# Kernel tuning notes

Measured on AMD Instinct MI355X. Metric: run time of the kernel, lower is better.

Reference implementation:

```python
import jax, jax.numpy as jnp
import numpy as np

NUM_NODES = 50000
EMB_DIM = 128
PROJ_DIM = 768
HIDDEN = 256
NUM_REL = 16
NUM_BASES = 2
NUM_LAYERS = 3
NUM_EDGES = 400000
BN_EPS = 1e-5


def setup_inputs() -> dict:
    key = jax.random.key(0)
    ks = jax.random.split(key, 32)
    inp = {}
    inp["edge_index"] = jax.random.randint(ks[0], (2, NUM_EDGES), 0, NUM_NODES)
    inp["edge_type"] = jax.random.randint(ks[1], (NUM_EDGES,), 0, NUM_REL)
    inp["emb"] = jax.random.normal(ks[2], (NUM_NODES, EMB_DIM), jnp.float32)
    inp["proj_w"] = jax.random.normal(ks[3], (EMB_DIM, PROJ_DIM), jnp.float32) * 0.02
    inp["proj_b"] = jnp.zeros((PROJ_DIM,), jnp.float32)
    dims_in = [PROJ_DIM, HIDDEN, HIDDEN]
    for l in range(NUM_LAYERS):
        d_in = dims_in[l]
        k0, k1, k2 = jax.random.split(ks[4 + l], 3)
        inp[f"comp{l}"] = jax.random.normal(k0, (NUM_REL, NUM_BASES), jnp.float32)
        inp[f"bases{l}"] = jax.random.normal(k1, (NUM_BASES, d_in, HIDDEN), jnp.float32) * (1.0 / np.sqrt(d_in))
        inp[f"root{l}"] = jax.random.normal(k2, (d_in, HIDDEN), jnp.float32) * (1.0 / np.sqrt(d_in))
        inp[f"bias{l}"] = jnp.zeros((HIDDEN,), jnp.float32)
        inp[f"gamma{l}"] = jnp.ones((HIDDEN,), jnp.float32)
        inp[f"beta{l}"] = jnp.zeros((HIDDEN,), jnp.float32)
    return inp


def _rgcn_conv(x, src, dst, edge_type, comp, bases, root, bias):
    # Basis decomposition: W_r = sum_b comp[r,b] * bases[b]
    # Transform nodes per basis once: [B, N, out]
    h = jnp.einsum('nd,bdo->bno', x, bases)
    c = comp[edge_type]                         # [E, B]
    msg = jnp.einsum('beo,eb->eo', h[:, src, :], c)  # [E, out]
    # PyG RGCNConv uses mean aggregation per relation
    seg = dst * NUM_REL + edge_type             # combined (node, relation) id
    cnt = jax.ops.segment_sum(jnp.ones((msg.shape[0],), x.dtype), seg,
                              num_segments=NUM_NODES * NUM_REL)
    denom = jnp.maximum(cnt[seg], 1.0)
    agg = jax.ops.segment_sum(msg / denom[:, None], dst, num_segments=NUM_NODES)
    return agg + x @ root + bias


def _batchnorm(x, gamma, beta):
    mu = jnp.mean(x, axis=0)
    var = jnp.mean(jnp.square(x - mu), axis=0)  # biased, as in torch BN training
    return (x - mu) * jax.lax.rsqrt(var + BN_EPS) * gamma + beta


def reference(edge_index, edge_type, emb, proj_w, proj_b,
              comp0, bases0, root0, bias0, gamma0, beta0,
              comp1, bases1, root1, bias1, gamma1, beta1,
              comp2, bases2, root2, bias2, gamma2, beta2):
    src, dst = edge_index[0], edge_index[1]
    x = emb / jnp.maximum(jnp.linalg.norm(emb, axis=-1, keepdims=True), 1e-12)
    x = x @ proj_w + proj_b
    layers = [(comp0, bases0, root0, bias0, gamma0, beta0),
              (comp1, bases1, root1, bias1, gamma1, beta1),
              (comp2, bases2, root2, bias2, gamma2, beta2)]
    for (comp, bases, root, bias, gamma, beta) in layers:
        x = _rgcn_conv(x, src, dst, edge_type, comp, bases, root, bias)
        x = _batchnorm(x, gamma, beta)
        x = jax.nn.relu(x)
        # dropout: identity (eval mode / deterministic reference)
    return x
```

## Files before the change

kernel.cpp:

```cpp
#include <hip/hip_runtime.h>
#include <hip/hip_bf16.h>

#define NNODES 50000
#define NREL   16
#define NEDGE  400000
#define BN_EPS 1e-5f
#define M_REAL NNODES
#define MT256  196
#define SCAN_B 512
#define SCAN_NB ((NNODES + SCAN_B - 1) / SCAN_B)

typedef __attribute__((ext_vector_type(8))) short short8;
typedef __attribute__((ext_vector_type(4))) float f4;

__device__ __forceinline__ float bf2f(unsigned short u) {
    union { unsigned int i; float f; } x; x.i = ((unsigned int)u) << 16; return x.f;
}
__device__ __forceinline__ unsigned short f2bf(float f) {
    __hip_bfloat16 h = __float2bfloat16(f);
    union { __hip_bfloat16 h; unsigned short u; } x; x.h = h; return x.u;
}

__device__ __forceinline__ void g2l16(const unsigned short* g, unsigned short* l) {
    __builtin_amdgcn_global_load_lds(
        (const __attribute__((address_space(1))) unsigned int*)g,
        (__attribute__((address_space(3))) unsigned int*)l,
        16, 0, 0);
}

template<int K>
__global__ __launch_bounds__(512) void gemm3_k(
    const unsigned short* __restrict__ A,
    const unsigned short* __restrict__ WT,
    const float* __restrict__ bias,
    unsigned short* __restrict__ y,
    float* __restrict__ bns)
{
    const int tile_m = blockIdx.x * 256;

    __shared__ unsigned short As[2][256 * 64];
    __shared__ unsigned short Bs[2][256 * 64];

    const int w = threadIdx.x >> 6;
    const int l = threadIdx.x & 63;
    const int lm = l & 15;
    const int kq = l >> 4;
    const int wm = (w & 1) << 7;
    const int wn = (w >> 1) << 6;

    const int lrow = l >> 3;
    const int chunk = ((l & 7) + 8 - lrow) & 7;
    const unsigned short* srcA[4];
    const unsigned short* srcB[4];
    int dstoff[4];
#pragma unroll
    for (int it = 0; it < 4; ++it) {
        int rt = it * 64 + w * 8 + lrow;
        int rg = tile_m + rt; if (rg >= M_REAL) rg = M_REAL - 1;
        srcA[it] = A  + (size_t)rg * K + chunk * 8;
        srcB[it] = WT + (size_t)rt * K + chunk * 8;
        dstoff[it] = (it * 64 + w * 8) * 64;
    }

    unsigned aoff[8], boff[4];
#pragma unroll
    for (int mi = 0; mi < 8; ++mi)
        aoff[mi] = (unsigned)((wm + mi * 16 + lm) * 128 + (((kq + lm) & 7) << 4));
#pragma unroll
    for (int ni = 0; ni < 4; ++ni)
        boff[ni] = (unsigned)((wn + ni * 16 + lm) * 128 + (((kq + lm) & 7) << 4));

    f4 acc[8][4];
#pragma unroll
    for (int mi = 0; mi < 8; ++mi)
#pragma unroll
        for (int ni = 0; ni < 4; ++ni) acc[mi][ni] = (f4){0.f, 0.f, 0.f, 0.f};

#pragma unroll
    for (int it = 0; it < 4; ++it) {
        g2l16(srcA[it], As[0] + dstoff[it]);
        g2l16(srcB[it], Bs[0] + dstoff[it]);
    }
    __syncthreads();

    int cur = 0;
    for (int kc = 0; kc < K; kc += 64) {
        if (kc + 64 < K) {
#pragma unroll
            for (int it = 0; it < 4; ++it) {
                g2l16(srcA[it] + kc + 64, As[cur ^ 1] + dstoff[it]);
                g2l16(srcB[it] + kc + 64, Bs[cur ^ 1] + dstoff[it]);
            }
        }
#pragma unroll
        for (int kh = 0; kh < 2; ++kh) {
            const unsigned x = kh << 6;
            short8 af[8], bfr[4];
#pragma unroll
            for (int mi = 0; mi < 8; ++mi)
                af[mi] = *(const short8*)((const char*)As[cur] + (aoff[mi] ^ x));
#pragma unroll
            for (int ni = 0; ni < 4; ++ni)
                bfr[ni] = *(const short8*)((const char*)Bs[cur] + (boff[ni] ^ x));
#pragma unroll
            for (int mi = 0; mi < 8; ++mi)
#pragma unroll
                for (int ni = 0; ni < 4; ++ni)
                    acc[mi][ni] = __builtin_amdgcn_mfma_f32_16x16x32_bf16(
                        af[mi], bfr[ni], acc[mi][ni], 0, 0, 0);
        }
        __syncthreads();
        cur ^= 1;
    }

    int cols[4]; float bv[4];
#pragma unroll
    for (int ni = 0; ni < 4; ++ni) {
        cols[ni] = wn + ni * 16 + lm;
        bv[ni] = bias[cols[ni]];
    }
    float s1[4] = {0.f, 0.f, 0.f, 0.f}, s2[4] = {0.f, 0.f, 0.f, 0.f};
#pragma unroll
    for (int mi = 0; mi < 8; ++mi) {
#pragma unroll
        for (int rg = 0; rg < 4; ++rg) {
            int row = tile_m + wm + mi * 16 + kq * 4 + rg;
            if (row < M_REAL) {
                size_t base = (size_t)row * 256;
#pragma unroll
                for (int ni = 0; ni < 4; ++ni) {
                    float v = acc[mi][ni][rg] + bv[ni];
                    y[base + cols[ni]] = f2bf(v);
                    s1[ni] += v; s2[ni] += v * v;
                }
            }
        }
    }
#pragma unroll
    for (int ni = 0; ni < 4; ++ni) {
        float a = s1[ni], b = s2[ni];
        a += __shfl_xor(a, 16); a += __shfl_xor(a, 32);
        b += __shfl_xor(b, 16); b += __shfl_xor(b, 32);
        if (l < 16) {
            atomicAdd(&bns[cols[ni]], a);
            atomicAdd(&bns[256 + cols[ni]], b);
        }
    }
}

template<int D, bool HAST>
__global__ __launch_bounds__(256) void gatheru_k(
    unsigned short* buf, const float* __restrict__ comp,
    const unsigned int* __restrict__ rowptr, const float2* __restrict__ erec)
{
    constexpr int E = D / 64;
    constexpr int S = 3 * D + (HAST ? 64 : 0);
    __shared__ float scomp[32];
    if (threadIdx.x < 32) scomp[threadIdx.x] = comp[threadIdx.x];
    __syncthreads();
    int node = blockIdx.x * 4 + (threadIdx.x >> 6);
    int lane = threadIdx.x & 63;
    unsigned int p0 = rowptr[node], p1 = rowptr[node + 1];
    const unsigned short* xbase = buf + 2 * D + lane * E;

    float a0[E], a1[E], b0[E], b1[E];
#pragma unroll
    for (int e = 0; e < E; ++e) { a0[e] = a1[e] = b0[e] = b1[e] = 0.f; }
    float t0 = 0.f, t1 = 0.f;

    unsigned int p = p0;
    for (; p + 4 <= p1; p += 4) {
        float2 r[4];
        unsigned short v[4][E];
#pragma unroll
        for (int j = 0; j < 4; ++j) r[j] = erec[p + j];
#pragma unroll
        for (int j = 0; j < 4; ++j) {
            unsigned q = __float_as_uint(r[j].x);
            const unsigned short* s = xbase + (size_t)(q >> 4) * S;
            if (E == 2) { ushort2 t = *(const ushort2*)s; v[j][0] = t.x; v[j][1] = t.y; }
            else        { ushort4 t = *(const ushort4*)s; v[j][0] = t.x; v[j][1] = t.y;
                          v[j][2] = t.z; v[j][3] = t.w; }
        }
#pragma unroll
        for (int j = 0; j < 4; ++j) {
            unsigned q = __float_as_uint(r[j].x);
            float w0 = scomp[(q & 15) * 2] * r[j].y;
            float w1 = scomp[(q & 15) * 2 + 1] * r[j].y;
            if (HAST) { t0 += w0; t1 += w1; }
            float* d0 = (j & 1) ? b0 : a0;
            float* d1 = (j & 1) ? b1 : a1;
#pragma unroll
            for (int e = 0; e < E; ++e) {
                float xv = bf2f(v[j][e]);
                d0[e] += w0 * xv;
                d1[e] += w1 * xv;
            }
        }
    }
    for (; p < p1; ++p) {
        float2 r = erec[p];
        unsigned q = __float_as_uint(r.x);
        const unsigned short* s = xbase + (size_t)(q >> 4) * S;
        unsigned short v[E];
        if (E == 2) { ushort2 t = *(const ushort2*)s; v[0] = t.x; v[1] = t.y; }
        else        { ushort4 t = *(const ushort4*)s; v[0] = t.x; v[1] = t.y;
                      v[2] = t.z; v[3] = t.w; }
        float w0 = scomp[(q & 15) * 2] * r.y;
        float w1 = scomp[(q & 15) * 2 + 1] * r.y;
        if (HAST) { t0 += w0; t1 += w1; }
#pragma unroll
        for (int e = 0; e < E; ++e) {
            float xv = bf2f(v[e]);
            a0[e] += w0 * xv;
            a1[e] += w1 * xv;
        }
    }

    unsigned short* orow = buf + (size_t)node * S;
    if (E == 2) {
        ushort2 o0, o1;
        o0.x = f2bf(a0[0] + b0[0]); o0.y = f2bf(a0[1] + b0[1]);
        o1.x = f2bf(a1[0] + b1[0]); o1.y = f2bf(a1[1] + b1[1]);
        *(ushort2*)(orow + lane * 2) = o0;
        *(ushort2*)(orow + D + lane * 2) = o1;
    } else {
        ushort4 o0, o1;
        o0.x = f2bf(a0[0] + b0[0]); o0.y = f2bf(a0[1] + b0[1]);
        o0.z = f2bf(a0[2] + b0[2]); o0.w = f2bf(a0[3] + b0[3]);
        o1.x = f2bf(a1[0] + b1[0]); o1.y = f2bf(a1[1] + b1[1]);
        o1.z = f2bf(a1[2] + b1[2]); o1.w = f2bf(a1[3] + b1[3]);
        *(ushort4*)(orow + lane * 4) = o0;
        *(ushort4*)(orow + D + lane * 4) = o1;
    }
    if (HAST) {
        unsigned short tv = (lane == 0) ? f2bf(t0) : (lane == 1) ? f2bf(t1) : (unsigned short)0;
        orow[3 * D + lane] = tv;
    }
}

__global__ __launch_bounds__(256) void norm_k(const float* __restrict__ emb,
                                              unsigned short* __restrict__ buf)
{
    int node = blockIdx.x * 4 + (threadIdx.x >> 6);
    int lane = threadIdx.x & 63;
    const float2* p = (const float2*)(emb + (size_t)node * 128);
    float2 v = p[lane];
    float ss = v.x * v.x + v.y * v.y;
#pragma unroll
    for (int o = 32; o > 0; o >>= 1) ss += __shfl_xor(ss, o);
    float inv = 1.f / fmaxf(sqrtf(ss), 1e-12f);
    unsigned short* row = buf + (size_t)node * 448 + 256;
    unsigned int pack = (unsigned int)f2bf(v.x * inv) | ((unsigned int)f2bf(v.y * inv) << 16);
    ((unsigned int*)row)[lane] = pack;
}

__global__ void zero_k(unsigned int* __restrict__ cnt, unsigned int* __restrict__ cntd,
                       unsigned int* __restrict__ cursor, float* __restrict__ bns)
{
    int i = blockIdx.x * 256 + threadIdx.x;
    if (i < 800000) cnt[i] = 0u;
    if (i < 50000) { cntd[i] = 0u; cursor[i] = 0u; }
    if (i < 1536) bns[i] = 0.f;
}

__global__ void cnt_k(const int* __restrict__ ei, const int* __restrict__ et,
                      unsigned int* __restrict__ cnt, unsigned int* __restrict__ cntd)
{
    int e = blockIdx.x * 256 + threadIdx.x;
    if (e >= NEDGE) return;
    int dst = ei[NEDGE + e];
    atomicAdd(&cnt[(size_t)dst * NREL + et[e]], 1u);
    atomicAdd(&cntd[dst], 1u);
}

__global__ __launch_bounds__(SCAN_B) void scan1_k(const unsigned int* __restrict__ cntd,
                                                  unsigned int* __restrict__ partial,
                                                  unsigned int* __restrict__ bsum)
{
    __shared__ unsigned int s[SCAN_B];
    int i = blockIdx.x * SCAN_B + threadIdx.x;
    unsigned int v = (i < NNODES) ? cntd[i] : 0u;
    s[threadIdx.x] = v;
    __syncthreads();
    for (int off = 1; off < SCAN_B; off <<= 1) {
        unsigned int t = (threadIdx.x >= off) ? s[threadIdx.x - off] : 0u;
        __syncthreads();
        s[threadIdx.x] += t;
        __syncthreads();
    }
    if (i < NNODES) partial[i] = s[threadIdx.x];
    if (threadIdx.x == SCAN_B - 1) bsum[blockIdx.x] = s[SCAN_B - 1];
}

__global__ __launch_bounds__(128) void scan2_k(unsigned int* __restrict__ bsum)
{
    __shared__ unsigned int s[128];
    unsigned int v = (threadIdx.x < SCAN_NB) ? bsum[threadIdx.x] : 0u;
    s[threadIdx.x] = v;
    __syncthreads();
    for (int off = 1; off < 128; off <<= 1) {
        unsigned int t = (threadIdx.x >= off) ? s[threadIdx.x - off] : 0u;
        __syncthreads();
        s[threadIdx.x] += t;
        __syncthreads();
    }
    if (threadIdx.x < SCAN_NB) bsum[threadIdx.x] = s[threadIdx.x];
}

__global__ __launch_bounds__(SCAN_B) void scan3_k(const unsigned int* __restrict__ partial,
                                                  const unsigned int* __restrict__ bsum,
                                                  unsigned int* __restrict__ rowptr)
{
    int i = blockIdx.x * SCAN_B + threadIdx.x;
    if (i >= NNODES) return;
    unsigned int off = (blockIdx.x > 0) ? bsum[blockIdx.x - 1] : 0u;
    rowptr[i + 1] = partial[i] + off;
    if (i == 0) rowptr[0] = 0u;
}

__global__ void fill_k(const int* __restrict__ ei, const int* __restrict__ et,
                       const unsigned int* __restrict__ cnt,
                       const unsigned int* __restrict__ rowptr,
                       unsigned int* __restrict__ cursor,
                       float2* __restrict__ erec)
{
    int e = blockIdx.x * 256 + threadIdx.x;
    if (e >= NEDGE) return;
    int dst = ei[NEDGE + e];
    int t = et[e];
    unsigned int c = cnt[(size_t)dst * NREL + t];
    unsigned int pos = rowptr[dst] + atomicAdd(&cursor[dst], 1u);
    float2 r;
    r.x = __uint_as_float(((unsigned)ei[e] << 4) | (unsigned)t);
    r.y = 1.f / (float)(c ? c : 1u);
    erec[pos] = r;
}

__global__ __launch_bounds__(128) void pt_k(const float* __restrict__ proj_w,
                                            float* __restrict__ PT)
{
    int j = blockIdx.x, d = threadIdx.x;
    PT[(size_t)j * 128 + d] = proj_w[(size_t)d * 768 + j];
}

__global__ __launch_bounds__(128) void pm_k(
    const float* __restrict__ PT, const float* __restrict__ pb,
    const float* __restrict__ b0, const float* __restrict__ r0,
    const float* __restrict__ bias0,
    unsigned short* __restrict__ wTm0, float* __restrict__ biasM0)
{
    __shared__ float sw[128];
    __shared__ float spb[128];
    __shared__ float red[2];
    int seg = blockIdx.x >> 8;
    int n = blockIdx.x & 255;
    int d = threadIdx.x;
    float acc = 0.f, accb = 0.f;
    for (int ch = 0; ch < 6; ++ch) {
        int j0 = ch * 128;
        __syncthreads();
        int j = j0 + d;
        float wv;
        if (seg == 0)      wv = b0[(size_t)j * 256 + n];
        else if (seg == 1) wv = b0[768 * 256 + (size_t)j * 256 + n];
        else               wv = r0[(size_t)j * 256 + n];
        sw[d] = wv;
        spb[d] = pb[j];
        __syncthreads();
#pragma unroll 8
        for (int jj = 0; jj < 128; ++jj)
            acc += PT[(size_t)(j0 + jj) * 128 + d] * sw[jj];
        accb += spb[d] * sw[d];
    }
    for (int o = 32; o > 0; o >>= 1) accb += __shfl_xor(accb, o);
    if ((d & 63) == 0) red[d >> 6] = accb;
    __syncthreads();
    float tb = red[0] + red[1];
    wTm0[(size_t)n * 448 + seg * 128 + d] = f2bf(acc);
    if (seg == 0) { if (d == 0) wTm0[(size_t)n * 448 + 384] = f2bf(tb); }
    else if (seg == 1) { if (d == 0) wTm0[(size_t)n * 448 + 385] = f2bf(tb); }
    else {
        if (d == 0) biasM0[n] = tb + bias0[n];
        if (d >= 2 && d < 64) wTm0[(size_t)n * 448 + 384 + d] = 0;
    }
}

__global__ __launch_bounds__(256) void prep_k(
    const float* __restrict__ b1, const float* __restrict__ r1, const float* __restrict__ bias1,
    const float* __restrict__ b2, const float* __restrict__ r2, const float* __restrict__ bias2,
    unsigned short* __restrict__ wTm1, unsigned short* __restrict__ wTm2,
    float* __restrict__ biasM1, float* __restrict__ biasM2)
{
    int b = blockIdx.x;
    int n = threadIdx.x;
    if (b < 1536) {
        int layer = b / 768;
        int rem = b % 768;
        int seg = rem / 256;
        int k = rem % 256;
        const float* bb = layer ? b2 : b1;
        const float* rr = layer ? r2 : r1;
        const float* in = (seg < 2) ? (bb + (size_t)seg * 256 * 256) : rr;
        unsigned short* out = layer ? wTm2 : wTm1;
        out[(size_t)n * 768 + seg * 256 + k] = f2bf(in[(size_t)k * 256 + n]);
    } else {
        int layer = b - 1536;
        float* bm = layer ? biasM2 : biasM1;
        const float* bs = layer ? bias2 : bias1;
        bm[n] = bs[n];
    }
}

template<bool LAST>
__global__ __launch_bounds__(256) void apply_k(const unsigned short* __restrict__ y,
                                               const float* __restrict__ bns,
                                               const float* __restrict__ gamma,
                                               const float* __restrict__ beta,
                                               unsigned short* __restrict__ xn,
                                               float* __restrict__ outp)
{
    __shared__ float scsh[512];
    {
        const float inv_m = 1.f / (float)M_REAL;
        int c = threadIdx.x;
        float m1 = bns[c] * inv_m;
        float var = fmaxf(bns[256 + c] * inv_m - m1 * m1, 0.f);
        float inv = rsqrtf(var + BN_EPS);
        float sc = gamma[c] * inv;
        scsh[c] = sc;
        scsh[256 + c] = beta[c] - m1 * sc;
    }
    __syncthreads();

    int i = blockIdx.x * 256 + threadIdx.x;
    int row = i >> 5;
    int c8 = (i & 31) * 8;
    short8 v = *(const short8*)(y + (size_t)row * 256 + c8);
    f4 sca = *(const f4*)&scsh[c8];
    f4 scb = *(const f4*)&scsh[c8 + 4];
    f4 sha = *(const f4*)&scsh[256 + c8];
    f4 shb = *(const f4*)&scsh[256 + c8 + 4];
    float o0 = fmaxf(bf2f((unsigned short)v[0]) * sca.x + sha.x, 0.f);
    float o1 = fmaxf(bf2f((unsigned short)v[1]) * sca.y + sha.y, 0.f);
    float o2 = fmaxf(bf2f((unsigned short)v[2]) * sca.z + sha.z, 0.f);
    float o3 = fmaxf(bf2f((unsigned short)v[3]) * sca.w + sha.w, 0.f);
    float o4 = fmaxf(bf2f((unsigned short)v[4]) * scb.x + shb.x, 0.f);
    float o5 = fmaxf(bf2f((unsigned short)v[5]) * scb.y + shb.y, 0.f);
    float o6 = fmaxf(bf2f((unsigned short)v[6]) * scb.z + shb.z, 0.f);
    float o7 = fmaxf(bf2f((unsigned short)v[7]) * scb.w + shb.w, 0.f);
    if (LAST) {
        f4 w0 = {o0, o1, o2, o3};
        f4 w1 = {o4, o5, o6, o7};
        float* dst = outp + (size_t)row * 256 + c8;
        *(f4*)dst = w0;
        *(f4*)(dst + 4) = w1;
    } else {
        short8 u;
        u[0] = (short)f2bf(o0); u[1] = (short)f2bf(o1);
        u[2] = (short)f2bf(o2); u[3] = (short)f2bf(o3);
        u[4] = (short)f2bf(o4); u[5] = (short)f2bf(o5);
        u[6] = (short)f2bf(o6); u[7] = (short)f2bf(o7);
        *(short8*)(xn + (size_t)row * 768 + 512 + c8) = u;
    }
}

extern "C" void kernel_launch(void* const* d_in, const int* in_sizes, int n_in,
                              void* d_out, int out_size, void* d_ws, size_t ws_size,
                              hipStream_t stream)
{
    const int*   edge_index = (const int*)d_in[0];
    const int*   edge_type  = (const int*)d_in[1];
    const float* emb    = (const float*)d_in[2];
    const float* proj_w = (const float*)d_in[3];
    const float* proj_b = (const float*)d_in[4];
    const float* comp[3]  = {(const float*)d_in[5],  (const float*)d_in[11], (const float*)d_in[17]};
    const float* bases[3] = {(const float*)d_in[6],  (const float*)d_in[12], (const float*)d_in[18]};
    const float* root[3]  = {(const float*)d_in[7],  (const float*)d_in[13], (const float*)d_in[19]};
    const float* biasp[3] = {(const float*)d_in[8],  (const float*)d_in[14], (const float*)d_in[20]};
    const float* gamma[3] = {(const float*)d_in[9],  (const float*)d_in[15], (const float*)d_in[21]};
    const float* beta[3]  = {(const float*)d_in[10], (const float*)d_in[16], (const float*)d_in[22]};

    char* ws = (char*)d_ws;
    size_t off = 0;
    auto alloc = [&](size_t bytes) -> char* {
        char* p = ws + off;
        off = (off + bytes + 255) & ~(size_t)255;
        return p;
    };

    unsigned short* axl0 = (unsigned short*)alloc((size_t)NNODES * 448 * 2);
    unsigned short* axl1 = (unsigned short*)alloc((size_t)NNODES * 768 * 2);
    unsigned short* axl2 = (unsigned short*)alloc((size_t)NNODES * 768 * 2);
    unsigned short* y    = (unsigned short*)alloc((size_t)NNODES * 256 * 2);
    unsigned int*   cnt  = (unsigned int*)alloc((size_t)NNODES * NREL * 4);
    unsigned int*   cntd = (unsigned int*)alloc((size_t)NNODES * 4);
    unsigned int*   rowptr = (unsigned int*)alloc((size_t)(NNODES + 1) * 4);
    unsigned int*   cursor = (unsigned int*)alloc((size_t)NNODES * 4);
    unsigned int*   partial = (unsigned int*)alloc((size_t)NNODES * 4);
    unsigned int*   bsum = (unsigned int*)alloc(128 * 4);
    float2*         erec = (float2*)alloc((size_t)NEDGE * 8);
    float*          PT   = (float*)alloc((size_t)768 * 128 * 4);
    unsigned short* wTm0 = (unsigned short*)alloc((size_t)256 * 448 * 2);
    unsigned short* wTm1 = (unsigned short*)alloc((size_t)256 * 768 * 2);
    unsigned short* wTm2 = (unsigned short*)alloc((size_t)256 * 768 * 2);
    float* biasM = (float*)alloc(3 * 256 * 4);
    float* bns   = (float*)alloc(3 * 512 * 4);

    zero_k<<<3125, 256, 0, stream>>>(cnt, cntd, cursor, bns);
    norm_k<<<NNODES / 4, 256, 0, stream>>>(emb, axl0);
    cnt_k<<<(NEDGE + 255) / 256, 256, 0, stream>>>(edge_index, edge_type, cnt, cntd);
    scan1_k<<<SCAN_NB, SCAN_B, 0, stream>>>(cntd, partial, bsum);
    scan2_k<<<1, 128, 0, stream>>>(bsum);
    scan3_k<<<SCAN_NB, SCAN_B, 0, stream>>>(partial, bsum, rowptr);
    fill_k<<<(NEDGE + 255) / 256, 256, 0, stream>>>(edge_index, edge_type, cnt, rowptr,
                                                    cursor, erec);

    pt_k<<<768, 128, 0, stream>>>(proj_w, PT);
    pm_k<<<768, 128, 0, stream>>>(PT, proj_b, bases[0], root[0], biasp[0], wTm0, biasM);
    prep_k<<<1538, 256, 0, stream>>>(bases[1], root[1], biasp[1],
                                     bases[2], root[2], biasp[2],
                                     wTm1, wTm2, biasM + 256, biasM + 512);

    gatheru_k<128, true><<<NNODES / 4, 256, 0, stream>>>(axl0, comp[0], rowptr, erec);
    gemm3_k<448><<<MT256, 512, 0, stream>>>(axl0, wTm0, biasM, y, bns);
    apply_k<false><<<(NNODES * 32) / 256, 256, 0, stream>>>(y, bns, gamma[0], beta[0],
                                                            axl1, nullptr);

    gatheru_k<256, false><<<NNODES / 4, 256, 0, stream>>>(axl1, comp[1], rowptr, erec);
    gemm3_k<768><<<MT256, 512, 0, stream>>>(axl1, wTm1, biasM + 256, y, bns + 512);
    apply_k<false><<<(NNODES * 32) / 256, 256, 0, stream>>>(y, bns + 512, gamma[1], beta[1],
                                                            axl2, nullptr);

    gatheru_k<256, false><<<NNODES / 4, 256, 0, stream>>>(axl2, comp[2], rowptr, erec);
    gemm3_k<768><<<MT256, 512, 0, stream>>>(axl2, wTm2, biasM + 512, y, bns + 1024);
    apply_k<true><<<(NNODES * 32) / 256, 256, 0, stream>>>(y, bns + 1024, gamma[2], beta[2],
                                                           nullptr, (float*)d_out);
}
```

Measured before the change: 483.5 us.

## Deepen GEMM pipeline to four-stage K=32 ring with explicit vmcnt waits

```diff
diff --git a/kernel.cpp b/kernel.cpp
--- a/kernel.cpp
+++ b/kernel.cpp
@@ -36,10 +36,11 @@
     unsigned short* __restrict__ y,
     float* __restrict__ bns)
 {
+    constexpr int NCH = K / 32;
     const int tile_m = blockIdx.x * 256;
 
-    __shared__ unsigned short As[2][256 * 64];
-    __shared__ unsigned short Bs[2][256 * 64];
+    __shared__ unsigned short As[4][256 * 32];
+    __shared__ unsigned short Bs[4][256 * 32];
 
     const int w = threadIdx.x >> 6;
     const int l = threadIdx.x & 63;
@@ -48,69 +49,80 @@
     const int wm = (w & 1) << 7;
     const int wn = (w >> 1) << 6;
 
-    const int lrow = l >> 3;
-    const int chunk = ((l & 7) + 8 - lrow) & 7;
-    const unsigned short* srcA[4];
-    const unsigned short* srcB[4];
-    int dstoff[4];
-#pragma unroll
-    for (int it = 0; it < 4; ++it) {
-        int rt = it * 64 + w * 8 + lrow;
+    const int srow = l >> 2;
+    const int schunk = ((l & 3) - ((l >> 3) & 3)) & 3;
+    unsigned aof[2], bof[2];
+    int dsto[2];
+#pragma unroll
+    for (int it = 0; it < 2; ++it) {
+        int rt = it * 128 + w * 16 + srow;
         int rg = tile_m + rt; if (rg >= M_REAL) rg = M_REAL - 1;
-        srcA[it] = A  + (size_t)rg * K + chunk * 8;
-        srcB[it] = WT + (size_t)rt * K + chunk * 8;
-        dstoff[it] = (it * 64 + w * 8) * 64;
+        aof[it] = (unsigned)rg * (unsigned)K + (unsigned)(schunk * 8);
+        bof[it] = (unsigned)rt * (unsigned)K + (unsigned)(schunk * 8);
+        dsto[it] = (it * 128 + w * 16) * 32;
     }
 
     unsigned aoff[8], boff[4];
 #pragma unroll
+    for (int mi = 0; mi < 8; ++mi) {
+        int r = wm + mi * 16 + lm;
+        aoff[mi] = (unsigned)(r * 64 + (((kq + ((lm >> 1) & 3)) & 3) << 4));
+    }
+#pragma unroll
+    for (int ni = 0; ni < 4; ++ni) {
+        int r = wn + ni * 16 + lm;
+        boff[ni] = (unsigned)(r * 64 + (((kq + ((lm >> 1) & 3)) & 3) << 4));
+    }
+
+    f4 acc[8][4];
+#pragma unroll
     for (int mi = 0; mi < 8; ++mi)
-        aoff[mi] = (unsigned)((wm + mi * 16 + lm) * 128 + (((kq + lm) & 7) << 4));
-#pragma unroll
-    for (int ni = 0; ni < 4; ++ni)
-        boff[ni] = (unsigned)((wn + ni * 16 + lm) * 128 + (((kq + lm) & 7) << 4));
-
-    f4 acc[8][4];
-#pragma unroll
-    for (int mi = 0; mi < 8; ++mi)
 #pragma unroll
         for (int ni = 0; ni < 4; ++ni) acc[mi][ni] = (f4){0.f, 0.f, 0.f, 0.f};
 
 #pragma unroll
-    for (int it = 0; it < 4; ++it) {
-        g2l16(srcA[it], As[0] + dstoff[it]);
-        g2l16(srcB[it], Bs[0] + dstoff[it]);
-    }
-    __syncthreads();
-
-    int cur = 0;
-    for (int kc = 0; kc < K; kc += 64) {
-        if (kc + 64 < K) {
-#pragma unroll
-            for (int it = 0; it < 4; ++it) {
-                g2l16(srcA[it] + kc + 64, As[cur ^ 1] + dstoff[it]);
-                g2l16(srcB[it] + kc + 64, Bs[cur ^ 1] + dstoff[it]);
+    for (int c0 = 0; c0 < 3; ++c0) {
+#pragma unroll
+        for (int it = 0; it < 2; ++it) {
+            g2l16(A + aof[it] + c0 * 32, As[c0] + dsto[it]);
+            g2l16(WT + bof[it] + c0 * 32, Bs[c0] + dsto[it]);
+        }
+    }
+
+    for (int c = 0; c < NCH; ++c) {
+        if (c < NCH - 2)
+            asm volatile("s_waitcnt vmcnt(8)" ::: "memory");
+        else if (c == NCH - 2)
+            asm volatile("s_waitcnt vmcnt(4)" ::: "memory");
+        else
+            asm volatile("s_waitcnt vmcnt(0)" ::: "memory");
+        __builtin_amdgcn_s_barrier();
+        __builtin_amdgcn_sched_barrier(0);
+
+        if (c + 3 < NCH) {
+            const int s = (c + 3) & 3;
+#pragma unroll
+            for (int it = 0; it < 2; ++it) {
+                g2l16(A + aof[it] + (c + 3) * 32, As[s] + dsto[it]);
+                g2l16(WT + bof[it] + (c + 3) * 32, Bs[s] + dsto[it]);
             }
         }
-#pragma unroll
-        for (int kh = 0; kh < 2; ++kh) {
-            const unsigned x = kh << 6;
-            short8 af[8], bfr[4];
-#pragma unroll
-            for (int mi = 0; mi < 8; ++mi)
-                af[mi] = *(const short8*)((const char*)As[cur] + (aoff[mi] ^ x));
+
+        const unsigned short* as = As[c & 3];
+        const unsigned short* bs = Bs[c & 3];
+        short8 af[8], bfr[4];
+#pragma unroll
+        for (int mi = 0; mi < 8; ++mi)
+            af[mi] = *(const short8*)((const char*)as + aoff[mi]);
+#pragma unroll
+        for (int ni = 0; ni < 4; ++ni)
+            bfr[ni] = *(const short8*)((const char*)bs + boff[ni]);
+#pragma unroll
+        for (int mi = 0; mi < 8; ++mi)
 #pragma unroll
             for (int ni = 0; ni < 4; ++ni)
-                bfr[ni] = *(const short8*)((const char*)Bs[cur] + (boff[ni] ^ x));
-#pragma unroll
-            for (int mi = 0; mi < 8; ++mi)
-#pragma unroll
-                for (int ni = 0; ni < 4; ++ni)
-                    acc[mi][ni] = __builtin_amdgcn_mfma_f32_16x16x32_bf16(
-                        af[mi], bfr[ni], acc[mi][ni], 0, 0, 0);
-        }
-        __syncthreads();
-        cur ^= 1;
+                acc[mi][ni] = __builtin_amdgcn_mfma_f32_16x16x32_bf16(
+                    af[mi], bfr[ni], acc[mi][ni], 0, 0, 0);
     }
 
     int cols[4]; float bv[4];
```

After: 502.3 us. 3.9% more time.

## Load GEMM weight fragments directly into registers instead of staging through LDS

Applied to the files above, without the earlier changes.

```diff
diff --git a/kernel.cpp b/kernel.cpp
--- a/kernel.cpp
+++ b/kernel.cpp
@@ -36,10 +36,10 @@
     unsigned short* __restrict__ y,
     float* __restrict__ bns)
 {
+    constexpr int NST = K / 64;
     const int tile_m = blockIdx.x * 256;
 
     __shared__ unsigned short As[2][256 * 64];
-    __shared__ unsigned short Bs[2][256 * 64];
 
     const int w = threadIdx.x >> 6;
     const int l = threadIdx.x & 63;
@@ -50,25 +50,24 @@
 
     const int lrow = l >> 3;
     const int chunk = ((l & 7) + 8 - lrow) & 7;
-    const unsigned short* srcA[4];
-    const unsigned short* srcB[4];
-    int dstoff[4];
+    unsigned aof[4]; int dsto[4];
 #pragma unroll
     for (int it = 0; it < 4; ++it) {
         int rt = it * 64 + w * 8 + lrow;
         int rg = tile_m + rt; if (rg >= M_REAL) rg = M_REAL - 1;
-        srcA[it] = A  + (size_t)rg * K + chunk * 8;
-        srcB[it] = WT + (size_t)rt * K + chunk * 8;
-        dstoff[it] = (it * 64 + w * 8) * 64;
-    }
-
-    unsigned aoff[8], boff[4];
+        aof[it] = (unsigned)rg * (unsigned)K + (unsigned)(chunk * 8);
+        dsto[it] = (it * 64 + w * 8) * 64;
+    }
+
+    unsigned aoff[8];
 #pragma unroll
     for (int mi = 0; mi < 8; ++mi)
         aoff[mi] = (unsigned)((wm + mi * 16 + lm) * 128 + (((kq + lm) & 7) << 4));
+
+    const unsigned short* wrow[4];
 #pragma unroll
     for (int ni = 0; ni < 4; ++ni)
-        boff[ni] = (unsigned)((wn + ni * 16 + lm) * 128 + (((kq + lm) & 7) << 4));
+        wrow[ni] = WT + (size_t)(wn + ni * 16 + lm) * K + kq * 8;
 
     f4 acc[8][4];
 #pragma unroll
@@ -77,40 +76,61 @@
         for (int ni = 0; ni < 4; ++ni) acc[mi][ni] = (f4){0.f, 0.f, 0.f, 0.f};
 
 #pragma unroll
-    for (int it = 0; it < 4; ++it) {
-        g2l16(srcA[it], As[0] + dstoff[it]);
-        g2l16(srcB[it], Bs[0] + dstoff[it]);
-    }
-    __syncthreads();
+    for (int it = 0; it < 4; ++it)
+        g2l16(A + aof[it], As[0] + dsto[it]);
+    short8 bcur[2][4];
+#pragma unroll
+    for (int kh = 0; kh < 2; ++kh)
+#pragma unroll
+        for (int ni = 0; ni < 4; ++ni)
+            bcur[kh][ni] = *(const short8*)(wrow[ni] + kh * 32);
+    asm volatile("s_waitcnt vmcnt(8)" ::: "memory");
+    __builtin_amdgcn_s_barrier();
+    __builtin_amdgcn_sched_barrier(0);
 
     int cur = 0;
-    for (int kc = 0; kc < K; kc += 64) {
-        if (kc + 64 < K) {
-#pragma unroll
-            for (int it = 0; it < 4; ++it) {
-                g2l16(srcA[it] + kc + 64, As[cur ^ 1] + dstoff[it]);
-                g2l16(srcB[it] + kc + 64, Bs[cur ^ 1] + dstoff[it]);
-            }
+#pragma unroll
+    for (int s = 0; s < NST; ++s) {
+        const int kc = s * 64;
+        const bool more = (s + 1 < NST);
+        short8 bnxt[2][4];
+        if (more) {
+#pragma unroll
+            for (int it = 0; it < 4; ++it)
+                g2l16(A + aof[it] + kc + 64, As[cur ^ 1] + dsto[it]);
+#pragma unroll
+            for (int kh = 0; kh < 2; ++kh)
+#pragma unroll
+                for (int ni = 0; ni < 4; ++ni)
+                    bnxt[kh][ni] = *(const short8*)(wrow[ni] + kc + 64 + kh * 32);
         }
 #pragma unroll
         for (int kh = 0; kh < 2; ++kh) {
             const unsigned x = kh << 6;
-            short8 af[8], bfr[4];
+            short8 af[8];
 #pragma unroll
             for (int mi = 0; mi < 8; ++mi)
                 af[mi] = *(const short8*)((const char*)As[cur] + (aoff[mi] ^ x));
 #pragma unroll
-            for (int ni = 0; ni < 4; ++ni)
-                bfr[ni] = *(const short8*)((const char*)Bs[cur] + (boff[ni] ^ x));
-#pragma unroll
             for (int mi = 0; mi < 8; ++mi)
 #pragma unroll
                 for (int ni = 0; ni < 4; ++ni)
                     acc[mi][ni] = __builtin_amdgcn_mfma_f32_16x16x32_bf16(
-                        af[mi], bfr[ni], acc[mi][ni], 0, 0, 0);
-        }
-        __syncthreads();
-        cur ^= 1;
+                        af[mi], bcur[kh][ni], acc[mi][ni], 0, 0, 0);
+        }
+        if (more) {
+            asm volatile("s_waitcnt lgkmcnt(0)" ::: "memory");
+            __builtin_amdgcn_sched_barrier(0);
+            asm volatile("s_waitcnt vmcnt(8)" ::: "memory");
+            __builtin_amdgcn_s_barrier();
+            __builtin_amdgcn_sched_barrier(0);
+#pragma unroll
+            for (int kh = 0; kh < 2; ++kh)
+#pragma unroll
+                for (int ni = 0; ni < 4; ++ni)
+                    bcur[kh][ni] = bnxt[kh][ni];
+            cur ^= 1;
+        }
     }
 
     int cols[4]; float bv[4];
```

Result: slower. 508.3 us (+5.1%).

## Use 224-row GEMM tiles to fill all CUs and merge small setup kernels

Applied to the files above, without the earlier changes.

```diff
diff --git a/kernel.cpp b/kernel.cpp
--- a/kernel.cpp
+++ b/kernel.cpp
@@ -6,7 +6,7 @@
 #define NEDGE  400000
 #define BN_EPS 1e-5f
 #define M_REAL NNODES
-#define MT256  196
+#define MT224  224
 #define SCAN_B 512
 #define SCAN_NB ((NNODES + SCAN_B - 1) / SCAN_B)
 
@@ -36,74 +36,84 @@
     unsigned short* __restrict__ y,
     float* __restrict__ bns)
 {
-    const int tile_m = blockIdx.x * 256;
-
-    __shared__ unsigned short As[2][256 * 64];
+    const int tile_m = blockIdx.x * 224;
+
+    __shared__ unsigned short As[2][224 * 64];
     __shared__ unsigned short Bs[2][256 * 64];
 
     const int w = threadIdx.x >> 6;
     const int l = threadIdx.x & 63;
     const int lm = l & 15;
     const int kq = l >> 4;
-    const int wm = (w & 1) << 7;
+    const int wm = (w & 1) * 112;
     const int wn = (w >> 1) << 6;
 
+    unsigned aof[4]; int dstA[4]; bool aact[4];
+#pragma unroll
+    for (int rnd = 0; rnd < 4; ++rnd) {
+        int c = (int)threadIdx.x + rnd * 512;
+        aact[rnd] = (c < 1792);
+        int cc = aact[rnd] ? c : 1791;
+        int row = cc >> 3, p = cc & 7;
+        int g = (p + 8 - (row & 7)) & 7;
+        int rg = tile_m + row; if (rg >= M_REAL) rg = M_REAL - 1;
+        aof[rnd] = (unsigned)rg * (unsigned)K + (unsigned)(g * 8);
+        dstA[rnd] = (w * 64 + rnd * 512) * 8;
+    }
     const int lrow = l >> 3;
     const int chunk = ((l & 7) + 8 - lrow) & 7;
-    const unsigned short* srcA[4];
-    const unsigned short* srcB[4];
-    int dstoff[4];
+    unsigned bof[4]; int dstB[4];
 #pragma unroll
     for (int it = 0; it < 4; ++it) {
         int rt = it * 64 + w * 8 + lrow;
-        int rg = tile_m + rt; if (rg >= M_REAL) rg = M_REAL - 1;
-        srcA[it] = A  + (size_t)rg * K + chunk * 8;
-        srcB[it] = WT + (size_t)rt * K + chunk * 8;
-        dstoff[it] = (it * 64 + w * 8) * 64;
-    }
-
-    unsigned aoff[8], boff[4];
-#pragma unroll
-    for (int mi = 0; mi < 8; ++mi)
+        bof[it] = (unsigned)rt * (unsigned)K + (unsigned)(chunk * 8);
+        dstB[it] = (it * 64 + w * 8) * 64;
+    }
+
+    unsigned aoff[7], boff[4];
+#pragma unroll
+    for (int mi = 0; mi < 7; ++mi)
         aoff[mi] = (unsigned)((wm + mi * 16 + lm) * 128 + (((kq + lm) & 7) << 4));
 #pragma unroll
     for (int ni = 0; ni < 4; ++ni)
         boff[ni] = (unsigned)((wn + ni * 16 + lm) * 128 + (((kq + lm) & 7) << 4));
 
-    f4 acc[8][4];
-#pragma unroll
-    for (int mi = 0; mi < 8; ++mi)
+    f4 acc[7][4];
+#pragma unroll
+    for (int mi = 0; mi < 7; ++mi)
 #pragma unroll
         for (int ni = 0; ni < 4; ++ni) acc[mi][ni] = (f4){0.f, 0.f, 0.f, 0.f};
 
 #pragma unroll
-    for (int it = 0; it < 4; ++it) {
-        g2l16(srcA[it], As[0] + dstoff[it]);
-        g2l16(srcB[it], Bs[0] + dstoff[it]);
-    }
+    for (int rnd = 0; rnd < 4; ++rnd)
+        if (aact[rnd]) g2l16(A + aof[rnd], As[0] + dstA[rnd]);
+#pragma unroll
+    for (int it = 0; it < 4; ++it)
+        g2l16(WT + bof[it], Bs[0] + dstB[it]);
     __syncthreads();
 
     int cur = 0;
     for (int kc = 0; kc < K; kc += 64) {
         if (kc + 64 < K) {
 #pragma unroll
-            for (int it = 0; it < 4; ++it) {
-                g2l16(srcA[it] + kc + 64, As[cur ^ 1] + dstoff[it]);
-                g2l16(srcB[it] + kc + 64, Bs[cur ^ 1] + dstoff[it]);
-            }
+            for (int rnd = 0; rnd < 4; ++rnd)
+                if (aact[rnd]) g2l16(A + aof[rnd] + kc + 64, As[cur ^ 1] + dstA[rnd]);
+#pragma unroll
+            for (int it = 0; it < 4; ++it)
+                g2l16(WT + bof[it] + kc + 64, Bs[cur ^ 1] + dstB[it]);
         }
 #pragma unroll
         for (int kh = 0; kh < 2; ++kh) {
             const unsigned x = kh << 6;
-            short8 af[8], bfr[4];
-#pragma unroll
-            for (int mi = 0; mi < 8; ++mi)
+            short8 af[7], bfr[4];
+#pragma unroll
+            for (int mi = 0; mi < 7; ++mi)
                 af[mi] = *(const short8*)((const char*)As[cur] + (aoff[mi] ^ x));
 #pragma unroll
             for (int ni = 0; ni < 4; ++ni)
                 bfr[ni] = *(const short8*)((const char*)Bs[cur] + (boff[ni] ^ x));
 #pragma unroll
-            for (int mi = 0; mi < 8; ++mi)
+            for (int mi = 0; mi < 7; ++mi)
 #pragma unroll
                 for (int ni = 0; ni < 4; ++ni)
                     acc[mi][ni] = __builtin_amdgcn_mfma_f32_16x16x32_bf16(
@@ -121,7 +131,7 @@
     }
     float s1[4] = {0.f, 0.f, 0.f, 0.f}, s2[4] = {0.f, 0.f, 0.f, 0.f};
 #pragma unroll
-    for (int mi = 0; mi < 8; ++mi) {
+    for (int mi = 0; mi < 7; ++mi) {
 #pragma unroll
         for (int rg = 0; rg < 4; ++rg) {
             int row = tile_m + wm + mi * 16 + kq * 4 + rg;
@@ -239,29 +249,29 @@
     }
 }
 
-__global__ __launch_bounds__(256) void norm_k(const float* __restrict__ emb,
-                                              unsigned short* __restrict__ buf)
-{
-    int node = blockIdx.x * 4 + (threadIdx.x >> 6);
-    int lane = threadIdx.x & 63;
-    const float2* p = (const float2*)(emb + (size_t)node * 128);
-    float2 v = p[lane];
-    float ss = v.x * v.x + v.y * v.y;
-#pragma unroll
-    for (int o = 32; o > 0; o >>= 1) ss += __shfl_xor(ss, o);
-    float inv = 1.f / fmaxf(sqrtf(ss), 1e-12f);
-    unsigned short* row = buf + (size_t)node * 448 + 256;
-    unsigned int pack = (unsigned int)f2bf(v.x * inv) | ((unsigned int)f2bf(v.y * inv) << 16);
-    ((unsigned int*)row)[lane] = pack;
-}
-
-__global__ void zero_k(unsigned int* __restrict__ cnt, unsigned int* __restrict__ cntd,
-                       unsigned int* __restrict__ cursor, float* __restrict__ bns)
-{
-    int i = blockIdx.x * 256 + threadIdx.x;
-    if (i < 800000) cnt[i] = 0u;
-    if (i < 50000) { cntd[i] = 0u; cursor[i] = 0u; }
-    if (i < 1536) bns[i] = 0.f;
+__global__ __launch_bounds__(256) void init_k(
+    unsigned int* __restrict__ cnt, unsigned int* __restrict__ cntd,
+    unsigned int* __restrict__ cursor, float* __restrict__ bns,
+    const float* __restrict__ emb, unsigned short* __restrict__ buf)
+{
+    if (blockIdx.x < 3125) {
+        int i = blockIdx.x * 256 + threadIdx.x;
+        if (i < 800000) cnt[i] = 0u;
+        if (i < 50000) { cntd[i] = 0u; cursor[i] = 0u; }
+        if (i < 1536) bns[i] = 0.f;
+    } else {
+        int node = (blockIdx.x - 3125) * 4 + (threadIdx.x >> 6);
+        int lane = threadIdx.x & 63;
+        const float2* p = (const float2*)(emb + (size_t)node * 128);
+        float2 v = p[lane];
+        float ss = v.x * v.x + v.y * v.y;
+#pragma unroll
+        for (int o = 32; o > 0; o >>= 1) ss += __shfl_xor(ss, o);
+        float inv = 1.f / fmaxf(sqrtf(ss), 1e-12f);
+        unsigned short* row = buf + (size_t)node * 448 + 256;
+        unsigned int pack = (unsigned int)f2bf(v.x * inv) | ((unsigned int)f2bf(v.y * inv) << 16);
+        ((unsigned int*)row)[lane] = pack;
+    }
 }
 
 __global__ void cnt_k(const int* __restrict__ ei, const int* __restrict__ et,
@@ -337,62 +347,21 @@
     erec[pos] = r;
 }
 
-__global__ __launch_bounds__(128) void pt_k(const float* __restrict__ proj_w,
-                                            float* __restrict__ PT)
-{
-    int j = blockIdx.x, d = threadIdx.x;
-    PT[(size_t)j * 128 + d] = proj_w[(size_t)d * 768 + j];
-}
-
-__global__ __launch_bounds__(128) void pm_k(
-    const float* __restrict__ PT, const float* __restrict__ pb,
-    const float* __restrict__ b0, const float* __restrict__ r0,
-    const float* __restrict__ bias0,
-    unsigned short* __restrict__ wTm0, float* __restrict__ biasM0)
-{
-    __shared__ float sw[128];
-    __shared__ float spb[128];
-    __shared__ float red[2];
-    int seg = blockIdx.x >> 8;
-    int n = blockIdx.x & 255;
-    int d = threadIdx.x;
-    float acc = 0.f, accb = 0.f;
-    for (int ch = 0; ch < 6; ++ch) {
-        int j0 = ch * 128;
-        __syncthreads();
-        int j = j0 + d;
-        float wv;
-        if (seg == 0)      wv = b0[(size_t)j * 256 + n];
-        else if (seg == 1) wv = b0[768 * 256 + (size_t)j * 256 + n];
-        else               wv = r0[(size_t)j * 256 + n];
-        sw[d] = wv;
-        spb[d] = pb[j];
-        __syncthreads();
-#pragma unroll 8
-        for (int jj = 0; jj < 128; ++jj)
-            acc += PT[(size_t)(j0 + jj) * 128 + d] * sw[jj];
-        accb += spb[d] * sw[d];
-    }
-    for (int o = 32; o > 0; o >>= 1) accb += __shfl_xor(accb, o);
-    if ((d & 63) == 0) red[d >> 6] = accb;
-    __syncthreads();
-    float tb = red[0] + red[1];
-    wTm0[(size_t)n * 448 + seg * 128 + d] = f2bf(acc);
-    if (seg == 0) { if (d == 0) wTm0[(size_t)n * 448 + 384] = f2bf(tb); }
-    else if (seg == 1) { if (d == 0) wTm0[(size_t)n * 448 + 385] = f2bf(tb); }
-    else {
-        if (d == 0) biasM0[n] = tb + bias0[n];
-        if (d >= 2 && d < 64) wTm0[(size_t)n * 448 + 384 + d] = 0;
-    }
-}
-
-__global__ __launch_bounds__(256) void prep_k(
+__global__ __launch_bounds__(256) void ptprep_k(
+    const float* __restrict__ proj_w, float* __restrict__ PT,
     const float* __restrict__ b1, const float* __restrict__ r1, const float* __restrict__ bias1,
     const float* __restrict__ b2, const float* __restrict__ r2, const float* __restrict__ bias2,
     unsigned short* __restrict__ wTm1, unsigned short* __restrict__ wTm2,
     float* __restrict__ biasM1, float* __restrict__ biasM2)
 {
     int b = blockIdx.x;
+    if (b < 384) {
+        int j = b * 2 + (threadIdx.x >> 7);
+        int d = threadIdx.x & 127;
+        PT[(size_t)j * 128 + d] = proj_w[(size_t)d * 768 + j];
+        return;
+    }
+    b -= 384;
     int n = threadIdx.x;
     if (b < 1536) {
         int layer = b / 768;
@@ -409,6 +378,48 @@
         float* bm = layer ? biasM2 : biasM1;
         const float* bs = layer ? bias2 : bias1;
         bm[n] = bs[n];
+    }
+}
+
+__global__ __launch_bounds__(128) void pm_k(
+    const float* __restrict__ PT, const float* __restrict__ pb,
+    const float* __restrict__ b0, const float* __restrict__ r0,
+    const float* __restrict__ bias0,
+    unsigned short* __restrict__ wTm0, float* __restrict__ biasM0)
+{
+    __shared__ float sw[128];
+    __shared__ float spb[128];
+    __shared__ float red[2];
+    int seg = blockIdx.x >> 8;
+    int n = blockIdx.x & 255;
+    int d = threadIdx.x;
+    float acc = 0.f, accb = 0.f;
+    for (int ch = 0; ch < 6; ++ch) {
+        int j0 = ch * 128;
+        __syncthreads();
+        int j = j0 + d;
+        float wv;
+        if (seg == 0)      wv = b0[(size_t)j * 256 + n];
+        else if (seg == 1) wv = b0[768 * 256 + (size_t)j * 256 + n];
+        else               wv = r0[(size_t)j * 256 + n];
+        sw[d] = wv;
+        spb[d] = pb[j];
+        __syncthreads();
+#pragma unroll 8
+        for (int jj = 0; jj < 128; ++jj)
+            acc += PT[(size_t)(j0 + jj) * 128 + d] * sw[jj];
+        accb += spb[d] * sw[d];
+    }
+    for (int o = 32; o > 0; o >>= 1) accb += __shfl_xor(accb, o);
+    if ((d & 63) == 0) red[d >> 6] = accb;
+    __syncthreads();
+    float tb = red[0] + red[1];
+    wTm0[(size_t)n * 448 + seg * 128 + d] = f2bf(acc);
+    if (seg == 0) { if (d == 0) wTm0[(size_t)n * 448 + 384] = f2bf(tb); }
+    else if (seg == 1) { if (d == 0) wTm0[(size_t)n * 448 + 385] = f2bf(tb); }
+    else {
+        if (d == 0) biasM0[n] = tb + bias0[n];
+        if (d >= 2 && d < 64) wTm0[(size_t)n * 448 + 384 + d] = 0;
     }
 }
 
@@ -507,8 +518,7 @@
     float* biasM = (float*)alloc(3 * 256 * 4);
     float* bns   = (float*)alloc(3 * 512 * 4);
 
-    zero_k<<<3125, 256, 0, stream>>>(cnt, cntd, cursor, bns);
-    norm_k<<<NNODES / 4, 256, 0, stream>>>(emb, axl0);
+    init_k<<<15625, 256, 0, stream>>>(cnt, cntd, cursor, bns, emb, axl0);
     cnt_k<<<(NEDGE + 255) / 256, 256, 0, stream>>>(edge_index, edge_type, cnt, cntd);
     scan1_k<<<SCAN_NB, SCAN_B, 0, stream>>>(cntd, partial, bsum);
     scan2_k<<<1, 128, 0, stream>>>(bsum);
@@ -516,24 +526,24 @@
     fill_k<<<(NEDGE + 255) / 256, 256, 0, stream>>>(edge_index, edge_type, cnt, rowptr,
                                                     cursor, erec);
 
-    pt_k<<<768, 128, 0, stream>>>(proj_w, PT);
+    ptprep_k<<<1922, 256, 0, stream>>>(proj_w, PT,
+                                       bases[1], root[1], biasp[1],
+                                       bases[2], root[2], biasp[2],
+                                       wTm1, wTm2, biasM + 256, biasM + 512);
     pm_k<<<768, 128, 0, stream>>>(PT, proj_b, bases[0], root[0], biasp[0], wTm0, biasM);
-    prep_k<<<1538, 256, 0, stream>>>(bases[1], root[1], biasp[1],
-                                     bases[2], root[2], biasp[2],
-                                     wTm1, wTm2, biasM + 256, biasM + 512);
 
     gatheru_k<128, true><<<NNODES / 4, 256, 0, stream>>>(axl0, comp[0], rowptr, erec);
-    gemm3_k<448><<<MT256, 512, 0, stream>>>(axl0, wTm0, biasM, y, bns);
+    gemm3_k<448><<<MT224, 512, 0, stream>>>(axl0, wTm0, biasM, y, bns);
     apply_k<false><<<(NNODES * 32) / 256, 256, 0, stream>>>(y, bns, gamma[0], beta[0],
                                                             axl1, nullptr);
 
     gatheru_k<256, false><<<NNODES / 4, 256, 0, stream>>>(axl1, comp[1], rowptr, erec);
-    gemm3_k<768><<<MT256, 512, 0, stream>>>(axl1, wTm1, biasM + 256, y, bns + 512);
+    gemm3_k<768><<<MT224, 512, 0, stream>>>(axl1, wTm1, biasM + 256, y, bns + 512);
     apply_k<false><<<(NNODES * 32) / 256, 256, 0, stream>>>(y, bns + 512, gamma[1], beta[1],
                                                             axl2, nullptr);
 
     gatheru_k<256, false><<<NNODES / 4, 256, 0, stream>>>(axl2, comp[2], rowptr, erec);
-    gemm3_k<768><<<MT256, 512, 0, stream>>>(axl2, wTm2, biasM + 512, y, bns + 1024);
+    gemm3_k<768><<<MT224, 512, 0, stream>>>(axl2, wTm2, biasM + 512, y, bns + 1024);
     apply_k<true><<<(NNODES * 32) / 256, 256, 0, stream>>>(y, bns + 1024, gamma[2], beta[2],
                                                            nullptr, (float*)d_out);
 }
```

Measured after the change: 488.8 us. About the same (+1.1%).
